# Kernel tuning notes

Hardware: AMD Instinct MI355X
Metric: run time of the kernel (lower is better)

## Reference

```python
import jax, jax.numpy as jnp
import numpy as np

B, S, D = 2, 2048, 1024
N_HEADS = 16
HEAD_DIM = D // N_HEADS  # 64, even for RoPE
THETA = 10000.0


def rope_tables(seq, head_dim, dtype=jnp.float32):
    half = head_dim // 2
    freqs = 1.0 / (THETA ** (jnp.arange(half, dtype=jnp.float32) / half))
    angles = jnp.arange(seq, dtype=jnp.float32)[:, None] * freqs[None, :]  # [S, half]
    return jnp.cos(angles).astype(dtype), jnp.sin(angles).astype(dtype)


def apply_rope_interleaved(x, cos, sin):
    # x: [b, h, s, d]; even/odd interleaving
    x_even = x[..., 0::2]
    x_odd = x[..., 1::2]
    r_even = x_even * cos - x_odd * sin
    r_odd = x_even * sin + x_odd * cos
    # interleave back: stack on last axis then reshape
    out = jnp.stack([r_even, r_odd], axis=-1).reshape(x.shape)
    return out


def setup_inputs() -> dict:
    key = jax.random.key(0)
    ks = jax.random.split(key, 6)
    scale = 1.0 / np.sqrt(D)
    return {
        "x": jax.random.normal(ks[0], (B, S, D), dtype=jnp.float32),
        "Wq": jax.random.normal(ks[1], (D, D), dtype=jnp.float32) * scale,
        "Wk": jax.random.normal(ks[2], (D, D), dtype=jnp.float32) * scale,
        "Wv": jax.random.normal(ks[3], (D, D), dtype=jnp.float32) * scale,
        "Wo": jax.random.normal(ks[4], (D, D), dtype=jnp.float32) * scale,
        "bo": jnp.zeros((D,), dtype=jnp.float32),
    }


def reference(x, Wq, Wk, Wv, Wo, bo):
    b, s, _ = x.shape
    # QKV projections (no bias), split heads -> [b, h, s, hd]
    def proj(W):
        return jnp.einsum('bsd,de->bse', x, W).reshape(b, s, N_HEADS, HEAD_DIM).transpose(0, 2, 1, 3)
    q, k, v = proj(Wq), proj(Wk), proj(Wv)

    cos, sin = rope_tables(s, HEAD_DIM, x.dtype)  # [s, hd//2]
    q = apply_rope_interleaved(q, cos, sin)
    k = apply_rope_interleaved(k, cos, sin)

    scale = 1.0 / jnp.sqrt(jnp.asarray(HEAD_DIM, dtype=x.dtype))
    scores = jnp.einsum('bhqd,bhkd->bhqk', q, k) * scale  # [b, h, s, s]
    causal = jnp.tril(jnp.ones((s, s), dtype=bool))
    scores = jnp.where(causal[None, None], scores, jnp.asarray(-jnp.inf, dtype=scores.dtype))
    attn = jax.nn.softmax(scores, axis=-1)
    ctx = jnp.einsum('bhqk,bhkd->bhqd', attn, v)  # [b, h, s, hd]
    ctx = ctx.transpose(0, 2, 1, 3).reshape(b, s, N_HEADS * HEAD_DIM)
    return jnp.einsum('bsd,de->bse', ctx, Wo) + bo
```

## Files before the change

kernel.cpp:

```cpp
#include <hip/hip_runtime.h>
#include <hip/hip_bf16.h>
#include <math.h>

constexpr int Bb   = 2;
constexpr int S    = 2048;
constexpr int D    = 1024;
constexpr int H    = 16;
constexpr int Dh   = 64;
constexpr int HALF = 32;
constexpr int M    = Bb * S;
constexpr int K    = 1024;
constexpr int N    = 1024;

typedef __attribute__((ext_vector_type(8))) short short8;
typedef __attribute__((ext_vector_type(4))) float f32x4;

__device__ __forceinline__ unsigned short f2bf(float f) {
    unsigned int u = __float_as_uint(f);
    unsigned int r = (u + 0x7fffu + ((u >> 16) & 1u)) >> 16;
    return (unsigned short)r;
}

__device__ __forceinline__ void gl_lds16(const unsigned short* g, unsigned short* lds_base) {
    __builtin_amdgcn_global_load_lds(
        (const __attribute__((address_space(1))) unsigned int*)g,
        (__attribute__((address_space(3))) unsigned int*)lds_base, 16, 0, 0);
}

__global__ __launch_bounds__(256) void prep_kernel(
    const float* __restrict__ x,
    const float* W0, const float* W1, const float* W2, const float* W3,
    unsigned short* __restrict__ xb,
    unsigned short* T0, unsigned short* T1, unsigned short* T2, unsigned short* T3,
    float* __restrict__ cosT, float* __restrict__ sinT)
{
    __shared__ float tile[64][65];
    const int bid = blockIdx.x;
    const int tid = threadIdx.x;

    if (bid < 256) {
        int idx = bid * 256 + tid;
        int s = idx >> 5;
        int i = idx & 31;
        double freq = exp(-(double)i * (log(10000.0) / 32.0));
        double ang  = (double)s * freq;
        cosT[idx] = (float)cos(ang);
        sinT[idx] = (float)sin(ang);
    } else if (bid < 256 + 4096) {
        size_t i = (size_t)(bid - 256) * 256 + tid;
        float4 v = *(const float4*)(x + i * 4);
        ushort4 pk;
        pk.x = f2bf(v.x); pk.y = f2bf(v.y); pk.z = f2bf(v.z); pk.w = f2bf(v.w);
        *(ushort4*)(xb + i * 4) = pk;
    } else {
        int wb = bid - 4352;
        int z  = wb >> 8;
        int rem = wb & 255;
        const float* W = (z == 0) ? W0 : (z == 1) ? W1 : (z == 2) ? W2 : W3;
        unsigned short* T = (z == 0) ? T0 : (z == 1) ? T1 : (z == 2) ? T2 : T3;
        const int bk = (rem >> 4) * 64;
        const int bn = (rem & 15) * 64;
        const int lr = tid >> 4;
        const int lc = (tid & 15) * 4;

        #pragma unroll
        for (int i = 0; i < 4; ++i) {
            int r = lr + i * 16;
            float4 v = *(const float4*)(W + (size_t)(bk + r) * N + bn + lc);
            tile[r][lc + 0] = v.x; tile[r][lc + 1] = v.y;
            tile[r][lc + 2] = v.z; tile[r][lc + 3] = v.w;
        }
        __syncthreads();
        #pragma unroll
        for (int i = 0; i < 4; ++i) {
            int nr = lr + i * 16;
            ushort4 pk;
            pk.x = f2bf(tile[lc + 0][nr]);
            pk.y = f2bf(tile[lc + 1][nr]);
            pk.z = f2bf(tile[lc + 2][nr]);
            pk.w = f2bf(tile[lc + 3][nr]);
            *(ushort4*)(T + (size_t)(bn + nr) * K + bk + lc) = pk;
        }
    }
}

__global__ __launch_bounds__(512, 2) void gemm_qkv_kernel(
    const unsigned short* __restrict__ A,
    const unsigned short* __restrict__ BT,
    unsigned short* outQ, unsigned short* outK, unsigned short* outV,
    const float* __restrict__ cosT, const float* __restrict__ sinT)
{
    constexpr int NT   = 32;
    constexpr int BUFS = 256 * 32;
    __shared__ __align__(16) unsigned short As[4 * BUFS];
    __shared__ __align__(16) unsigned short Bs[4 * BUFS];

    const int tid  = threadIdx.x;
    const int wid  = tid >> 6;
    const int lane = tid & 63;
    const int col  = lane & 15;
    const int quad = lane >> 4;
    const int wr   = wid >> 2;
    const int wc   = wid & 3;

    const int mbase = blockIdx.y * 256;
    const int nbase = blockIdx.x * 256;

    const int srow = lane >> 2;
    const int sch  = lane & 3;
    const unsigned short *pA0, *pA1, *pB0, *pB1;
    unsigned short *dA0, *dA1, *dB0, *dB1;
    {
        int r0 = wid * 16 + srow;
        int r1 = 128 + wid * 16 + srow;
        pA0 = A  + (size_t)(mbase + r0) * K + ((sch + (r0 >> 1)) & 3) * 8;
        pA1 = A  + (size_t)(mbase + r1) * K + ((sch + (r1 >> 1)) & 3) * 8;
        pB0 = BT + (size_t)(nbase + r0) * K + ((sch + (r0 >> 1)) & 3) * 8;
        pB1 = BT + (size_t)(nbase + r1) * K + ((sch + (r1 >> 1)) & 3) * 8;
        dA0 = &As[(wid * 16) * 32];
        dA1 = &As[(128 + wid * 16) * 32];
        dB0 = &Bs[(wid * 16) * 32];
        dB1 = &Bs[(128 + wid * 16) * 32];
    }

    int aoff[8], boff[4];
    #pragma unroll
    for (int f = 0; f < 8; ++f) {
        int r = wr * 128 + f * 16 + col;
        aoff[f] = r * 32 + ((quad - (r >> 1)) & 3) * 8;
    }
    #pragma unroll
    for (int n = 0; n < 4; ++n) {
        int r = wc * 64 + n * 16 + col;
        boff[n] = r * 32 + ((quad - (r >> 1)) & 3) * 8;
    }

    f32x4 acc[8][4];
    #pragma unroll
    for (int f = 0; f < 8; ++f)
        #pragma unroll
        for (int n = 0; n < 4; ++n) acc[f][n] = (f32x4)0.f;

    auto stageA = [&](int slot) {
        gl_lds16(pA0, dA0 + slot * BUFS); pA0 += 32;
        gl_lds16(pA1, dA1 + slot * BUFS); pA1 += 32;
    };
    auto stageB = [&](int slot) {
        gl_lds16(pB0, dB0 + slot * BUFS); pB0 += 32;
        gl_lds16(pB1, dB1 + slot * BUFS); pB1 += 32;
    };

    stageA(0); stageB(0);
    stageA(1); stageB(1);
    stageA(2); stageB(2);
    asm volatile("s_waitcnt vmcnt(8)" ::: "memory");
    __builtin_amdgcn_s_barrier();
    __builtin_amdgcn_sched_barrier(0);

    #pragma unroll 1
    for (int t = 0; t < NT; ++t) {
        const unsigned short* Ab = &As[(t & 3) * BUFS];
        const unsigned short* Bc = &Bs[(t & 3) * BUFS];
        const int nslot = (t + 3) & 3;
        short8 af[4], bf[4];

        #pragma unroll
        for (int i = 0; i < 4; ++i) af[i] = *(const short8*)&Ab[aoff[i]];
        #pragma unroll
        for (int n = 0; n < 4; ++n) bf[n] = *(const short8*)&Bc[boff[n]];
        if (t < NT - 3) stageA(nslot);
        __builtin_amdgcn_sched_barrier(0);
        __builtin_amdgcn_s_barrier();
        asm volatile("s_waitcnt lgkmcnt(0)" ::: "memory");
        __builtin_amdgcn_s_setprio(1);
        #pragma unroll
        for (int i = 0; i < 4; ++i)
            #pragma unroll
            for (int n = 0; n < 4; ++n)
                acc[i][n] = __builtin_amdgcn_mfma_f32_16x16x32_bf16(af[i], bf[n], acc[i][n], 0, 0, 0);
        __builtin_amdgcn_s_setprio(0);
        __builtin_amdgcn_sched_barrier(0);
        __builtin_amdgcn_s_barrier();
        __builtin_amdgcn_sched_barrier(0);

        #pragma unroll
        for (int i = 0; i < 4; ++i) af[i] = *(const short8*)&Ab[aoff[4 + i]];
        if (t < NT - 3) stageB(nslot);
        __builtin_amdgcn_sched_barrier(0);
        __builtin_amdgcn_s_barrier();
        asm volatile("s_waitcnt lgkmcnt(0)" ::: "memory");
        __builtin_amdgcn_s_setprio(1);
        #pragma unroll
        for (int i = 0; i < 4; ++i)
            #pragma unroll
            for (int n = 0; n < 4; ++n)
                acc[4 + i][n] = __builtin_amdgcn_mfma_f32_16x16x32_bf16(af[i], bf[n], acc[4 + i][n], 0, 0, 0);
        __builtin_amdgcn_s_setprio(0);
        if (t < NT - 3)       { asm volatile("s_waitcnt vmcnt(8)" ::: "memory"); }
        else if (t == NT - 3) { asm volatile("s_waitcnt vmcnt(4)" ::: "memory"); }
        else if (t == NT - 2) { asm volatile("s_waitcnt vmcnt(0)" ::: "memory"); }
        __builtin_amdgcn_s_barrier();
        __builtin_amdgcn_sched_barrier(0);
    }

    const int z = nbase >> 10;
    if (z < 2) {
        unsigned short* o = z ? outK : outQ;
        #pragma unroll
        for (int n = 0; n < 4; ++n) {
            int nl = (nbase & 1023) + wc * 64 + n * 16 + col;
            int h = nl >> 6, dh0 = nl & 63, p = dh0 >> 1;
            bool even = !(dh0 & 1);
            #pragma unroll
            for (int f = 0; f < 8; ++f)
                #pragma unroll
                for (int reg = 0; reg < 4; ++reg) {
                    int m_g = mbase + wr * 128 + f * 16 + quad * 4 + reg;
                    int b = m_g >> 11, s = m_g & 2047;
                    float v = acc[f][n][reg];
                    float part = __shfl_xor(v, 1, 64);
                    float c = cosT[s * HALF + p], sn = sinT[s * HALF + p];
                    float r = even ? (v * c - part * sn) : (v * c + part * sn);
                    o[((size_t)(b * H + h) * S + s) * Dh + dh0] = f2bf(r);
                }
        }
    } else {
        #pragma unroll
        for (int n = 0; n < 4; ++n) {
            int nl = (nbase & 1023) + wc * 64 + n * 16 + col;
            int h = nl >> 6, dh0 = nl & 63;
            #pragma unroll
            for (int f = 0; f < 8; ++f) {
                int m0 = mbase + wr * 128 + f * 16 + quad * 4;
                int b = m0 >> 11, s = m0 & 2047;
                ushort4 pk;
                pk.x = f2bf(acc[f][n][0]);
                pk.y = f2bf(acc[f][n][1]);
                pk.z = f2bf(acc[f][n][2]);
                pk.w = f2bf(acc[f][n][3]);
                *(ushort4*)&outV[((size_t)(b * H + h) * Dh + dh0) * S + s] = pk;
            }
        }
    }
}

__global__ __launch_bounds__(256) void gemm_out_kernel(
    const unsigned short* __restrict__ A,
    const unsigned short* __restrict__ BT,
    float* __restrict__ outO, const float* __restrict__ bias)
{
    constexpr int BK   = 64;
    constexpr int ABUF = 64 * BK;
    constexpr int BBUF = 64 * BK;
    __shared__ __align__(16) unsigned short As[2 * ABUF];
    __shared__ __align__(16) unsigned short Bs[2 * BBUF];

    const int tid  = threadIdx.x;
    const int wave = tid >> 6;
    const int lane = tid & 63;
    const int col  = lane & 15;
    const int quad = lane >> 4;
    const int wy   = wave >> 1;
    const int wx   = wave & 1;

    const int mbase = blockIdx.y * 64;
    const int nbase = blockIdx.x * 64;

    const int srow8 = lane >> 3;
    const int sch8  = lane & 7;

    const unsigned short *pA[2], *pB[2];
    unsigned short *dA[2], *dB[2];
    #pragma unroll
    for (int w = 0; w < 2; ++w) {
        int base = wave * 16 + w * 8;
        int tr = base + srow8;
        pA[w] = A  + (size_t)(mbase + tr) * K + ((sch8 + (tr >> 1)) & 7) * 8;
        pB[w] = BT + (size_t)(nbase + tr) * K + ((sch8 + (tr >> 1)) & 7) * 8;
        dA[w] = &As[base * BK];
        dB[w] = &Bs[base * BK];
    }

    int aoff[2][2], boff[2][2];
    #pragma unroll
    for (int ks = 0; ks < 2; ++ks) {
        #pragma unroll
        for (int mi = 0; mi < 2; ++mi) {
            int r = wy * 32 + mi * 16 + col;
            aoff[ks][mi] = r * BK + (((ks * 4 + quad) - (r >> 1)) & 7) * 8;
        }
        #pragma unroll
        for (int ni = 0; ni < 2; ++ni) {
            int r = wx * 32 + ni * 16 + col;
            boff[ks][ni] = r * BK + (((ks * 4 + quad) - (r >> 1)) & 7) * 8;
        }
    }

    f32x4 acc[2][2];
    #pragma unroll
    for (int mi = 0; mi < 2; ++mi)
        #pragma unroll
        for (int ni = 0; ni < 2; ++ni) acc[mi][ni] = (f32x4)0.f;

    auto stage = [&](int buf) {
        #pragma unroll
        for (int w = 0; w < 2; ++w) { gl_lds16(pA[w], dA[w] + buf * ABUF); pA[w] += BK; }
        #pragma unroll
        for (int w = 0; w < 2; ++w) { gl_lds16(pB[w], dB[w] + buf * BBUF); pB[w] += BK; }
    };
    auto compute = [&](int buf) {
        const unsigned short* Ac = &As[buf * ABUF];
        const unsigned short* Bc = &Bs[buf * BBUF];
        #pragma unroll
        for (int ks = 0; ks < 2; ++ks) {
            short8 af[2], bfr[2];
            #pragma unroll
            for (int mi = 0; mi < 2; ++mi) af[mi] = *(const short8*)&Ac[aoff[ks][mi]];
            #pragma unroll
            for (int ni = 0; ni < 2; ++ni) bfr[ni] = *(const short8*)&Bc[boff[ks][ni]];
            #pragma unroll
            for (int mi = 0; mi < 2; ++mi)
                #pragma unroll
                for (int ni = 0; ni < 2; ++ni)
                    acc[mi][ni] = __builtin_amdgcn_mfma_f32_16x16x32_bf16(af[mi], bfr[ni], acc[mi][ni], 0, 0, 0);
        }
    };

    stage(0);
    #pragma unroll 1
    for (int kk = 0; kk < 16; kk += 2) {
        __syncthreads();
        if (kk + 1 < 16) stage(1);
        compute(0);
        __syncthreads();
        if (kk + 2 < 16) stage(0);
        compute(1);
    }

    #pragma unroll
    for (int ni = 0; ni < 2; ++ni) {
        int n_g = nbase + wx * 32 + ni * 16 + col;
        float bv = bias[n_g];
        #pragma unroll
        for (int mi = 0; mi < 2; ++mi)
            #pragma unroll
            for (int reg = 0; reg < 4; ++reg) {
                int m_g = mbase + wy * 32 + mi * 16 + quad * 4 + reg;
                outO[(size_t)m_g * N + n_g] = acc[mi][ni][reg] + bv;
            }
    }
}

__global__ __launch_bounds__(256) void attn_mfma_kernel(
    const unsigned short* __restrict__ q, const unsigned short* __restrict__ k,
    const unsigned short* __restrict__ vt,
    float* __restrict__ Opart, float* __restrict__ lpart)
{
    constexpr int TSZ = 64 * 64;
    __shared__ __align__(16) unsigned short Ks[2 * TSZ];
    __shared__ __align__(16) unsigned short Vs[2 * TSZ];
    __shared__ __align__(16) unsigned short Ps[4][16 * 64];

    const int tid  = threadIdx.x;
    const int wave = tid >> 6;
    const int lane = tid & 63;
    const int col  = lane & 15;
    const int quad = lane >> 4;
    const int l8   = lane >> 3, cp = lane & 7;

    const int pairh = blockIdx.x;
    const int pair  = pairh >> 1;
    const int hpar  = pairh & 1;
    const int bh = blockIdx.y;
    const unsigned short* qb = q  + (size_t)bh * S * Dh;
    const unsigned short* kb = k  + (size_t)bh * S * Dh;
    const unsigned short* vb = vt + (size_t)bh * Dh * S;

    unsigned short* dk0 = &Ks[(wave * 16 + 0) * 64];
    unsigned short* dk1 = &Ks[(wave * 16 + 8) * 64];
    unsigned short* dv0 = &Vs[(wave * 16 + 0) * 64];
    unsigned short* dv1 = &Vs[(wave * 16 + 8) * 64];

    int foff[2][4];
    #pragma unroll
    for (int ks = 0; ks < 2; ++ks)
        #pragma unroll
        for (int nt = 0; nt < 4; ++nt) {
            int r = nt * 16 + col;
            foff[ks][nt] = r * 64 + (((ks * 4 + quad) - r) & 7) * 8;
        }
    int poffW[4][4];
    #pragma unroll
    for (int nt = 0; nt < 4; ++nt)
        #pragma unroll
        for (int reg = 0; reg < 4; ++reg) {
            int row = quad * 4 + reg;
            poffW[nt][reg] = row * 64 + (((nt * 2 + (col >> 3)) ^ (row & 7)) << 3) + (col & 7);
        }
    int poffR[2];
    #pragma unroll
    for (int ks = 0; ks < 2; ++ks)
        poffR[ks] = col * 64 + (((ks * 4 + quad) ^ (col & 7)) << 3);

    for (int phase = 0; phase < 2; ++phase) {
        const int qt  = phase ? (31 - pair) : pair;
        const int wr0 = qt * 64 + wave * 16;

        const unsigned short *pk0, *pk1, *pv0, *pv1;
        {
            int r0 = wave * 16 + l8, r1 = r0 + 8;
            pk0 = kb + (size_t)(hpar * 64 + r0) * Dh + ((cp + r0) & 7) * 8;
            pk1 = kb + (size_t)(hpar * 64 + r1) * Dh + ((cp + r1) & 7) * 8;
            pv0 = vb + (size_t)r0 * S + hpar * 64 + ((cp + r0) & 7) * 8;
            pv1 = vb + (size_t)r1 * S + hpar * 64 + ((cp + r1) & 7) * 8;
        }

        auto stageKV = [&](int buf) {
            gl_lds16(pk0, dk0 + buf * TSZ); gl_lds16(pk1, dk1 + buf * TSZ);
            gl_lds16(pv0, dv0 + buf * TSZ); gl_lds16(pv1, dv1 + buf * TSZ);
            pk0 += 128 * Dh; pk1 += 128 * Dh; pv0 += 128; pv1 += 128;
        };

        __syncthreads();
        if (hpar <= qt) stageKV(0);

        short8 qfrag[2];
        #pragma unroll
        for (int ks = 0; ks < 2; ++ks)
            qfrag[ks] = *(const short8*)(qb + (size_t)(wr0 + col) * Dh + ks * 32 + quad * 8);

        f32x4 O[4];
        float lacc[4];
        #pragma unroll
        for (int nt = 0; nt < 4; ++nt) O[nt] = (f32x4)0.f;
        #pragma unroll
        for (int r = 0; r < 4; ++r) lacc[r] = 0.f;

        auto subtile = [&](const unsigned short* Kc, const unsigned short* Vc, int t) {
            f32x4 sacc[4];
            #pragma unroll
            for (int nt = 0; nt < 4; ++nt) sacc[nt] = (f32x4)0.f;
            #pragma unroll
            for (int ks = 0; ks < 2; ++ks)
                #pragma unroll
                for (int nt = 0; nt < 4; ++nt) {
                    short8 kf = *(const short8*)&Kc[foff[ks][nt]];
                    sacc[nt] = __builtin_amdgcn_mfma_f32_16x16x32_bf16(qfrag[ks], kf, sacc[nt], 0, 0, 0);
                }
            float pb[4][4];
            #pragma unroll
            for (int nt = 0; nt < 4; ++nt) {
                int key_l = nt * 16 + col;
                #pragma unroll
                for (int reg = 0; reg < 4; ++reg) {
                    float e = __builtin_amdgcn_exp2f(
                        fmaf(sacc[nt][reg], 0.18033688011112042f, -11.541560327111707f));
                    if (t == qt && key_l > wave * 16 + quad * 4 + reg) e = 0.f;
                    pb[nt][reg] = e;
                }
            }
            #pragma unroll
            for (int reg = 0; reg < 4; ++reg)
                lacc[reg] += (pb[0][reg] + pb[1][reg]) + (pb[2][reg] + pb[3][reg]);
            #pragma unroll
            for (int nt = 0; nt < 4; ++nt)
                #pragma unroll
                for (int reg = 0; reg < 4; ++reg)
                    Ps[wave][poffW[nt][reg]] = f2bf(pb[nt][reg]);
            #pragma unroll
            for (int ks = 0; ks < 2; ++ks) {
                short8 pf = *(const short8*)&Ps[wave][poffR[ks]];
                #pragma unroll
                for (int nt = 0; nt < 4; ++nt) {
                    short8 vf = *(const short8*)&Vc[foff[ks][nt]];
                    O[nt] = __builtin_amdgcn_mfma_f32_16x16x32_bf16(pf, vf, O[nt], 0, 0, 0);
                }
            }
        };

        int j = 0;
        for (int i = hpar; i <= qt; i += 2, ++j) {
            __syncthreads();
            if (i + 2 <= qt) stageKV((j + 1) & 1);
            subtile(&Ks[(j & 1) * TSZ], &Vs[(j & 1) * TSZ], i);
        }

        #pragma unroll
        for (int reg = 0; reg < 4; ++reg) {
            float s = lacc[reg];
            #pragma unroll
            for (int off = 1; off <= 8; off <<= 1)
                s += __shfl_xor(s, off, 64);
            lacc[reg] = s;
        }

        const size_t pb_base = (size_t)(hpar * 32 + bh) * S;
        #pragma unroll
        for (int reg = 0; reg < 4; ++reg) {
            int rg = wr0 + quad * 4 + reg;
            float* op = Opart + (pb_base + rg) * 64 + col;
            #pragma unroll
            for (int nt = 0; nt < 4; ++nt)
                op[nt * 16] = O[nt][reg];
            if (col == 0)
                lpart[pb_base + rg] = lacc[reg];
        }
    }
}

__global__ __launch_bounds__(256) void combine_kernel(
    const float* __restrict__ Opart, const float* __restrict__ lpart,
    unsigned short* __restrict__ ctx)
{
    int gid = blockIdx.x * 256 + threadIdx.x;
    int bh  = gid >> 15;
    int rem = gid & 32767;
    int qr  = rem >> 4;
    int dg  = (rem & 15) << 2;

    size_t i0 = ((size_t)bh * S + qr) * 64 + dg;
    size_t i1 = ((size_t)(32 + bh) * S + qr) * 64 + dg;
    float4 a = *(const float4*)(Opart + i0);
    float4 c = *(const float4*)(Opart + i1);
    float inv = 1.0f / (lpart[(size_t)bh * S + qr] + lpart[(size_t)(32 + bh) * S + qr]);

    int b = bh >> 4, hh = bh & 15;
    ushort4 pk;
    pk.x = f2bf((a.x + c.x) * inv);
    pk.y = f2bf((a.y + c.y) * inv);
    pk.z = f2bf((a.z + c.z) * inv);
    pk.w = f2bf((a.w + c.w) * inv);
    *(ushort4*)(ctx + ((size_t)b * S + qr) * 1024 + hh * 64 + dg) = pk;
}

extern "C" void kernel_launch(void* const* d_in, const int* in_sizes, int n_in,
                              void* d_out, int out_size, void* d_ws, size_t ws_size,
                              hipStream_t stream) {
    const float* x  = (const float*)d_in[0];
    const float* Wq = (const float*)d_in[1];
    const float* Wk = (const float*)d_in[2];
    const float* Wv = (const float*)d_in[3];
    const float* Wo = (const float*)d_in[4];
    const float* bo = (const float*)d_in[5];
    float* out = (float*)d_out;

    const size_t MK  = (size_t)M * K;
    const size_t NK  = (size_t)N * K;
    const size_t QKV = (size_t)Bb * H * S * Dh;

    unsigned short* xb   = (unsigned short*)d_ws;
    unsigned short* WqT  = xb  + MK;
    unsigned short* WkT  = WqT + NK;
    unsigned short* WvT  = WkT + NK;
    unsigned short* WoT  = WvT + NK;
    unsigned short* qbuf = WoT + NK;
    unsigned short* kbuf = qbuf + QKV;
    unsigned short* vtb  = kbuf + QKV;
    unsigned short* ctxb = vtb  + QKV;
    float* cosT  = (float*)(ctxb + QKV);
    float* sinT  = cosT + (size_t)S * HALF;
    float* Opart = sinT + (size_t)S * HALF;
    float* lpart = Opart + (size_t)2 * 32 * S * 64;

    prep_kernel<<<5376, 256, 0, stream>>>(x, Wq, Wk, Wv, Wo,
                                          xb, WqT, WkT, WvT, WoT, cosT, sinT);

    gemm_qkv_kernel<<<dim3(12, 16), 512, 0, stream>>>(
        xb, WqT, qbuf, kbuf, vtb, cosT, sinT);

    attn_mfma_kernel<<<dim3(32, Bb * H), 256, 0, stream>>>(qbuf, kbuf, vtb, Opart, lpart);

    combine_kernel<<<4096, 256, 0, stream>>>(Opart, lpart, ctxb);

    gemm_out_kernel<<<dim3(16, 64), 256, 0, stream>>>(ctxb, WoT, out, bo);
}
```

Measured before the change: 188.8 us.

## Shrink QKV GEMM to 128x128 tiles with simple double buffering

Replaces the 256x256-tile, 512-thread QKV GEMM with 128x128 tiles, 256 threads and a plain two-buffer pipeline that uses __syncthreads. The old version had a 4-stage pipeline with hand-placed waitcnt, setprio and sched barriers. The grid grows from 192 to 768 blocks, which should fill the 256 CUs better and cut wave-quantization tail. In exchange, each block reuses less data per tile, and the loads no longer overlap compute as finely, so global and LDS traffic per FLOP rises.

```diff
diff --git a/kernel.cpp b/kernel.cpp
--- a/kernel.cpp
+++ b/kernel.cpp
@@ -84,140 +84,109 @@
     }
 }
 
-__global__ __launch_bounds__(512, 2) void gemm_qkv_kernel(
+__global__ __launch_bounds__(256) void gemm_qkv_kernel(
     const unsigned short* __restrict__ A,
     const unsigned short* __restrict__ BT,
     unsigned short* outQ, unsigned short* outK, unsigned short* outV,
     const float* __restrict__ cosT, const float* __restrict__ sinT)
 {
-    constexpr int NT   = 32;
-    constexpr int BUFS = 256 * 32;
-    __shared__ __align__(16) unsigned short As[4 * BUFS];
-    __shared__ __align__(16) unsigned short Bs[4 * BUFS];
+    constexpr int BUF = 128 * 32;
+    __shared__ __align__(16) unsigned short As[2 * BUF];
+    __shared__ __align__(16) unsigned short Bs[2 * BUF];
 
     const int tid  = threadIdx.x;
-    const int wid  = tid >> 6;
+    const int wave = tid >> 6;
     const int lane = tid & 63;
     const int col  = lane & 15;
     const int quad = lane >> 4;
-    const int wr   = wid >> 2;
-    const int wc   = wid & 3;
-
-    const int mbase = blockIdx.y * 256;
-    const int nbase = blockIdx.x * 256;
+    const int wy   = wave >> 1;
+    const int wx   = wave & 1;
+
+    const int mbase = blockIdx.y * 128;
+    const int nbase = blockIdx.x * 128;
 
     const int srow = lane >> 2;
     const int sch  = lane & 3;
     const unsigned short *pA0, *pA1, *pB0, *pB1;
     unsigned short *dA0, *dA1, *dB0, *dB1;
     {
-        int r0 = wid * 16 + srow;
-        int r1 = 128 + wid * 16 + srow;
+        int r0 = wave * 32 + srow;
+        int r1 = wave * 32 + 16 + srow;
         pA0 = A  + (size_t)(mbase + r0) * K + ((sch + (r0 >> 1)) & 3) * 8;
         pA1 = A  + (size_t)(mbase + r1) * K + ((sch + (r1 >> 1)) & 3) * 8;
         pB0 = BT + (size_t)(nbase + r0) * K + ((sch + (r0 >> 1)) & 3) * 8;
         pB1 = BT + (size_t)(nbase + r1) * K + ((sch + (r1 >> 1)) & 3) * 8;
-        dA0 = &As[(wid * 16) * 32];
-        dA1 = &As[(128 + wid * 16) * 32];
-        dB0 = &Bs[(wid * 16) * 32];
-        dB1 = &Bs[(128 + wid * 16) * 32];
-    }
-
-    int aoff[8], boff[4];
-    #pragma unroll
-    for (int f = 0; f < 8; ++f) {
-        int r = wr * 128 + f * 16 + col;
-        aoff[f] = r * 32 + ((quad - (r >> 1)) & 3) * 8;
-    }
-    #pragma unroll
-    for (int n = 0; n < 4; ++n) {
-        int r = wc * 64 + n * 16 + col;
-        boff[n] = r * 32 + ((quad - (r >> 1)) & 3) * 8;
-    }
-
-    f32x4 acc[8][4];
-    #pragma unroll
-    for (int f = 0; f < 8; ++f)
-        #pragma unroll
-        for (int n = 0; n < 4; ++n) acc[f][n] = (f32x4)0.f;
-
-    auto stageA = [&](int slot) {
-        gl_lds16(pA0, dA0 + slot * BUFS); pA0 += 32;
-        gl_lds16(pA1, dA1 + slot * BUFS); pA1 += 32;
+        dA0 = &As[(wave * 32) * 32];
+        dA1 = &As[(wave * 32 + 16) * 32];
+        dB0 = &Bs[(wave * 32) * 32];
+        dB1 = &Bs[(wave * 32 + 16) * 32];
+    }
+
+    int aoff[4], boff[4];
+    #pragma unroll
+    for (int mi = 0; mi < 4; ++mi) {
+        int r = wy * 64 + mi * 16 + col;
+        aoff[mi] = r * 32 + ((quad - (r >> 1)) & 3) * 8;
+    }
+    #pragma unroll
+    for (int ni = 0; ni < 4; ++ni) {
+        int r = wx * 64 + ni * 16 + col;
+        boff[ni] = r * 32 + ((quad - (r >> 1)) & 3) * 8;
+    }
+
+    f32x4 acc[4][4];
+    #pragma unroll
+    for (int mi = 0; mi < 4; ++mi)
+        #pragma unroll
+        for (int ni = 0; ni < 4; ++ni) acc[mi][ni] = (f32x4)0.f;
+
+    auto stage = [&](int buf) {
+        gl_lds16(pA0, dA0 + buf * BUF);  pA0 += 32;
+        gl_lds16(pA1, dA1 + buf * BUF);  pA1 += 32;
+        gl_lds16(pB0, dB0 + buf * BUF);  pB0 += 32;
+        gl_lds16(pB1, dB1 + buf * BUF);  pB1 += 32;
     };
-    auto stageB = [&](int slot) {
-        gl_lds16(pB0, dB0 + slot * BUFS); pB0 += 32;
-        gl_lds16(pB1, dB1 + slot * BUFS); pB1 += 32;
+    auto compute = [&](int buf) {
+        const unsigned short* Ac = &As[buf * BUF];
+        const unsigned short* Bc = &Bs[buf * BUF];
+        short8 af[4], bfr[4];
+        #pragma unroll
+        for (int mi = 0; mi < 4; ++mi) af[mi] = *(const short8*)&Ac[aoff[mi]];
+        #pragma unroll
+        for (int ni = 0; ni < 4; ++ni) bfr[ni] = *(const short8*)&Bc[boff[ni]];
+        #pragma unroll
+        for (int mi = 0; mi < 4; ++mi)
+            #pragma unroll
+            for (int ni = 0; ni < 4; ++ni)
+                acc[mi][ni] = __builtin_amdgcn_mfma_f32_16x16x32_bf16(af[mi], bfr[ni], acc[mi][ni], 0, 0, 0);
     };
 
-    stageA(0); stageB(0);
-    stageA(1); stageB(1);
-    stageA(2); stageB(2);
-    asm volatile("s_waitcnt vmcnt(8)" ::: "memory");
-    __builtin_amdgcn_s_barrier();
-    __builtin_amdgcn_sched_barrier(0);
-
+    stage(0);
     #pragma unroll 1
-    for (int t = 0; t < NT; ++t) {
-        const unsigned short* Ab = &As[(t & 3) * BUFS];
-        const unsigned short* Bc = &Bs[(t & 3) * BUFS];
-        const int nslot = (t + 3) & 3;
-        short8 af[4], bf[4];
-
-        #pragma unroll
-        for (int i = 0; i < 4; ++i) af[i] = *(const short8*)&Ab[aoff[i]];
-        #pragma unroll
-        for (int n = 0; n < 4; ++n) bf[n] = *(const short8*)&Bc[boff[n]];
-        if (t < NT - 3) stageA(nslot);
-        __builtin_amdgcn_sched_barrier(0);
-        __builtin_amdgcn_s_barrier();
-        asm volatile("s_waitcnt lgkmcnt(0)" ::: "memory");
-        __builtin_amdgcn_s_setprio(1);
-        #pragma unroll
-        for (int i = 0; i < 4; ++i)
-            #pragma unroll
-            for (int n = 0; n < 4; ++n)
-                acc[i][n] = __builtin_amdgcn_mfma_f32_16x16x32_bf16(af[i], bf[n], acc[i][n], 0, 0, 0);
-        __builtin_amdgcn_s_setprio(0);
-        __builtin_amdgcn_sched_barrier(0);
-        __builtin_amdgcn_s_barrier();
-        __builtin_amdgcn_sched_barrier(0);
-
-        #pragma unroll
-        for (int i = 0; i < 4; ++i) af[i] = *(const short8*)&Ab[aoff[4 + i]];
-        if (t < NT - 3) stageB(nslot);
-        __builtin_amdgcn_sched_barrier(0);
-        __builtin_amdgcn_s_barrier();
-        asm volatile("s_waitcnt lgkmcnt(0)" ::: "memory");
-        __builtin_amdgcn_s_setprio(1);
-        #pragma unroll
-        for (int i = 0; i < 4; ++i)
-            #pragma unroll
-            for (int n = 0; n < 4; ++n)
-                acc[4 + i][n] = __builtin_amdgcn_mfma_f32_16x16x32_bf16(af[i], bf[n], acc[4 + i][n], 0, 0, 0);
-        __builtin_amdgcn_s_setprio(0);
-        if (t < NT - 3)       { asm volatile("s_waitcnt vmcnt(8)" ::: "memory"); }
-        else if (t == NT - 3) { asm volatile("s_waitcnt vmcnt(4)" ::: "memory"); }
-        else if (t == NT - 2) { asm volatile("s_waitcnt vmcnt(0)" ::: "memory"); }
-        __builtin_amdgcn_s_barrier();
-        __builtin_amdgcn_sched_barrier(0);
+    for (int kk = 0; kk < 32; kk += 2) {
+        __syncthreads();
+        if (kk + 1 < 32) stage(1);
+        compute(0);
+        __syncthreads();
+        if (kk + 2 < 32) stage(0);
+        compute(1);
     }
 
     const int z = nbase >> 10;
     if (z < 2) {
         unsigned short* o = z ? outK : outQ;
         #pragma unroll
-        for (int n = 0; n < 4; ++n) {
-            int nl = (nbase & 1023) + wc * 64 + n * 16 + col;
+        for (int ni = 0; ni < 4; ++ni) {
+            int nl = (nbase & 1023) + wx * 64 + ni * 16 + col;
             int h = nl >> 6, dh0 = nl & 63, p = dh0 >> 1;
             bool even = !(dh0 & 1);
             #pragma unroll
-            for (int f = 0; f < 8; ++f)
+            for (int mi = 0; mi < 4; ++mi)
                 #pragma unroll
                 for (int reg = 0; reg < 4; ++reg) {
-                    int m_g = mbase + wr * 128 + f * 16 + quad * 4 + reg;
+                    int m_g = mbase + wy * 64 + mi * 16 + quad * 4 + reg;
                     int b = m_g >> 11, s = m_g & 2047;
-                    float v = acc[f][n][reg];
+                    float v = acc[mi][ni][reg];
                     float part = __shfl_xor(v, 1, 64);
                     float c = cosT[s * HALF + p], sn = sinT[s * HALF + p];
                     float r = even ? (v * c - part * sn) : (v * c + part * sn);
@@ -226,18 +195,18 @@
         }
     } else {
         #pragma unroll
-        for (int n = 0; n < 4; ++n) {
-            int nl = (nbase & 1023) + wc * 64 + n * 16 + col;
+        for (int ni = 0; ni < 4; ++ni) {
+            int nl = (nbase & 1023) + wx * 64 + ni * 16 + col;
             int h = nl >> 6, dh0 = nl & 63;
             #pragma unroll
-            for (int f = 0; f < 8; ++f) {
-                int m0 = mbase + wr * 128 + f * 16 + quad * 4;
+            for (int mi = 0; mi < 4; ++mi) {
+                int m0 = mbase + wy * 64 + mi * 16 + quad * 4;
                 int b = m0 >> 11, s = m0 & 2047;
                 ushort4 pk;
-                pk.x = f2bf(acc[f][n][0]);
-                pk.y = f2bf(acc[f][n][1]);
-                pk.z = f2bf(acc[f][n][2]);
-                pk.w = f2bf(acc[f][n][3]);
+                pk.x = f2bf(acc[mi][ni][0]);
+                pk.y = f2bf(acc[mi][ni][1]);
+                pk.z = f2bf(acc[mi][ni][2]);
+                pk.w = f2bf(acc[mi][ni][3]);
                 *(ushort4*)&outV[((size_t)(b * H + h) * Dh + dh0) * S + s] = pk;
             }
         }
@@ -565,7 +534,7 @@
     prep_kernel<<<5376, 256, 0, stream>>>(x, Wq, Wk, Wv, Wo,
                                           xb, WqT, WkT, WvT, WoT, cosT, sinT);
 
-    gemm_qkv_kernel<<<dim3(12, 16), 512, 0, stream>>>(
+    gemm_qkv_kernel<<<dim3(24, 32), 256, 0, stream>>>(
         xb, WqT, qbuf, kbuf, vtb, cosT, sinT);
 
     attn_mfma_kernel<<<dim3(32, Bb * H), 256, 0, stream>>>(qbuf, kbuf, vtb, Opart, lpart);
```

Result: slower. 199.3 us (+5.6%).

## Retile QKV GEMM to 256x192 tiles with K=64 double buffering

Applied to the files above, without the earlier changes.

The QKV projection GEMM now uses 256x192 output tiles instead of 256x256, so the grid grows from 192 to 256 workgroups and better fills the GPU's compute units. The K step doubles to 64 per stage with two LDS slots instead of a four-deep ring of K=32 slots, and the swizzle is widened to 8 chunks. Because the tile no longer lines up with the Q/K/V 1024 boundaries, the epilogue picks the output and RoPE path per column group. The shallower pipeline waits for all loads (vmcnt(0)) each iteration, which may expose more memory latency.

```diff
diff --git a/kernel.cpp b/kernel.cpp
--- a/kernel.cpp
+++ b/kernel.cpp
@@ -90,10 +90,11 @@
     unsigned short* outQ, unsigned short* outK, unsigned short* outV,
     const float* __restrict__ cosT, const float* __restrict__ sinT)
 {
-    constexpr int NT   = 32;
-    constexpr int BUFS = 256 * 32;
-    __shared__ __align__(16) unsigned short As[4 * BUFS];
-    __shared__ __align__(16) unsigned short Bs[4 * BUFS];
+    constexpr int NT    = 16;
+    constexpr int ASLOT = 256 * 64;
+    constexpr int BSLOT = 192 * 64;
+    __shared__ __align__(16) unsigned short As[2 * ASLOT];
+    __shared__ __align__(16) unsigned short Bs[2 * BSLOT];
 
     const int tid  = threadIdx.x;
     const int wid  = tid >> 6;
@@ -104,71 +105,72 @@
     const int wc   = wid & 3;
 
     const int mbase = blockIdx.y * 256;
-    const int nbase = blockIdx.x * 256;
-
-    const int srow = lane >> 2;
-    const int sch  = lane & 3;
-    const unsigned short *pA0, *pA1, *pB0, *pB1;
-    unsigned short *dA0, *dA1, *dB0, *dB1;
-    {
-        int r0 = wid * 16 + srow;
-        int r1 = 128 + wid * 16 + srow;
-        pA0 = A  + (size_t)(mbase + r0) * K + ((sch + (r0 >> 1)) & 3) * 8;
-        pA1 = A  + (size_t)(mbase + r1) * K + ((sch + (r1 >> 1)) & 3) * 8;
-        pB0 = BT + (size_t)(nbase + r0) * K + ((sch + (r0 >> 1)) & 3) * 8;
-        pB1 = BT + (size_t)(nbase + r1) * K + ((sch + (r1 >> 1)) & 3) * 8;
-        dA0 = &As[(wid * 16) * 32];
-        dA1 = &As[(128 + wid * 16) * 32];
-        dB0 = &Bs[(wid * 16) * 32];
-        dB1 = &Bs[(128 + wid * 16) * 32];
-    }
-
-    int aoff[8], boff[4];
-    #pragma unroll
-    for (int f = 0; f < 8; ++f) {
-        int r = wr * 128 + f * 16 + col;
-        aoff[f] = r * 32 + ((quad - (r >> 1)) & 3) * 8;
-    }
-    #pragma unroll
-    for (int n = 0; n < 4; ++n) {
-        int r = wc * 64 + n * 16 + col;
-        boff[n] = r * 32 + ((quad - (r >> 1)) & 3) * 8;
-    }
-
-    f32x4 acc[8][4];
+    const int nbase = blockIdx.x * 192;
+
+    const int srow8 = lane >> 3;
+    const int sch8  = lane & 7;
+    const unsigned short *pA[4], *pB[3];
+    unsigned short *dA[4], *dB[3];
+    #pragma unroll
+    for (int w = 0; w < 4; ++w) {
+        int r = wid * 32 + w * 8 + srow8;
+        pA[w] = A + (size_t)(mbase + r) * K + ((sch8 + (r >> 1)) & 7) * 8;
+        dA[w] = &As[(wid * 32 + w * 8) * 64];
+    }
+    #pragma unroll
+    for (int w = 0; w < 3; ++w) {
+        int r = wid * 24 + w * 8 + srow8;
+        pB[w] = BT + (size_t)(nbase + r) * K + ((sch8 + (r >> 1)) & 7) * 8;
+        dB[w] = &Bs[(wid * 24 + w * 8) * 64];
+    }
+
+    int aoff[2][8], boff[2][3];
+    #pragma unroll
+    for (int kh = 0; kh < 2; ++kh) {
+        #pragma unroll
+        for (int f = 0; f < 8; ++f) {
+            int r = wr * 128 + f * 16 + col;
+            aoff[kh][f] = r * 64 + (((kh * 4 + quad) - (r >> 1)) & 7) * 8;
+        }
+        #pragma unroll
+        for (int n = 0; n < 3; ++n) {
+            int r = wc * 48 + n * 16 + col;
+            boff[kh][n] = r * 64 + (((kh * 4 + quad) - (r >> 1)) & 7) * 8;
+        }
+    }
+
+    f32x4 acc[8][3];
     #pragma unroll
     for (int f = 0; f < 8; ++f)
         #pragma unroll
-        for (int n = 0; n < 4; ++n) acc[f][n] = (f32x4)0.f;
+        for (int n = 0; n < 3; ++n) acc[f][n] = (f32x4)0.f;
 
     auto stageA = [&](int slot) {
-        gl_lds16(pA0, dA0 + slot * BUFS); pA0 += 32;
-        gl_lds16(pA1, dA1 + slot * BUFS); pA1 += 32;
+        #pragma unroll
+        for (int w = 0; w < 4; ++w) { gl_lds16(pA[w], dA[w] + slot * ASLOT); pA[w] += 64; }
     };
     auto stageB = [&](int slot) {
-        gl_lds16(pB0, dB0 + slot * BUFS); pB0 += 32;
-        gl_lds16(pB1, dB1 + slot * BUFS); pB1 += 32;
+        #pragma unroll
+        for (int w = 0; w < 3; ++w) { gl_lds16(pB[w], dB[w] + slot * BSLOT); pB[w] += 64; }
     };
 
     stageA(0); stageB(0);
-    stageA(1); stageB(1);
-    stageA(2); stageB(2);
-    asm volatile("s_waitcnt vmcnt(8)" ::: "memory");
+    asm volatile("s_waitcnt vmcnt(0)" ::: "memory");
     __builtin_amdgcn_s_barrier();
     __builtin_amdgcn_sched_barrier(0);
 
     #pragma unroll 1
     for (int t = 0; t < NT; ++t) {
-        const unsigned short* Ab = &As[(t & 3) * BUFS];
-        const unsigned short* Bc = &Bs[(t & 3) * BUFS];
-        const int nslot = (t + 3) & 3;
-        short8 af[4], bf[4];
-
-        #pragma unroll
-        for (int i = 0; i < 4; ++i) af[i] = *(const short8*)&Ab[aoff[i]];
-        #pragma unroll
-        for (int n = 0; n < 4; ++n) bf[n] = *(const short8*)&Bc[boff[n]];
-        if (t < NT - 3) stageA(nslot);
+        const unsigned short* Ab = &As[(t & 1) * ASLOT];
+        const unsigned short* Bc = &Bs[(t & 1) * BSLOT];
+        const int ns = (t + 1) & 1;
+        short8 af[4], bf[3];
+
+        #pragma unroll
+        for (int i = 0; i < 4; ++i) af[i] = *(const short8*)&Ab[aoff[0][i]];
+        #pragma unroll
+        for (int n = 0; n < 3; ++n) bf[n] = *(const short8*)&Bc[boff[0][n]];
+        if (t < NT - 1) stageA(ns);
         __builtin_amdgcn_sched_barrier(0);
         __builtin_amdgcn_s_barrier();
         asm volatile("s_waitcnt lgkmcnt(0)" ::: "memory");
@@ -176,7 +178,7 @@
         #pragma unroll
         for (int i = 0; i < 4; ++i)
             #pragma unroll
-            for (int n = 0; n < 4; ++n)
+            for (int n = 0; n < 3; ++n)
                 acc[i][n] = __builtin_amdgcn_mfma_f32_16x16x32_bf16(af[i], bf[n], acc[i][n], 0, 0, 0);
         __builtin_amdgcn_s_setprio(0);
         __builtin_amdgcn_sched_barrier(0);
@@ -184,8 +186,8 @@
         __builtin_amdgcn_sched_barrier(0);
 
         #pragma unroll
-        for (int i = 0; i < 4; ++i) af[i] = *(const short8*)&Ab[aoff[4 + i]];
-        if (t < NT - 3) stageB(nslot);
+        for (int i = 0; i < 4; ++i) af[i] = *(const short8*)&Ab[aoff[0][4 + i]];
+        if (t < NT - 1) stageB(ns);
         __builtin_amdgcn_sched_barrier(0);
         __builtin_amdgcn_s_barrier();
         asm volatile("s_waitcnt lgkmcnt(0)" ::: "memory");
@@ -193,23 +195,58 @@
         #pragma unroll
         for (int i = 0; i < 4; ++i)
             #pragma unroll
-            for (int n = 0; n < 4; ++n)
+            for (int n = 0; n < 3; ++n)
                 acc[4 + i][n] = __builtin_amdgcn_mfma_f32_16x16x32_bf16(af[i], bf[n], acc[4 + i][n], 0, 0, 0);
         __builtin_amdgcn_s_setprio(0);
-        if (t < NT - 3)       { asm volatile("s_waitcnt vmcnt(8)" ::: "memory"); }
-        else if (t == NT - 3) { asm volatile("s_waitcnt vmcnt(4)" ::: "memory"); }
-        else if (t == NT - 2) { asm volatile("s_waitcnt vmcnt(0)" ::: "memory"); }
-        __builtin_amdgcn_s_barrier();
-        __builtin_amdgcn_sched_barrier(0);
-    }
-
-    const int z = nbase >> 10;
-    if (z < 2) {
-        unsigned short* o = z ? outK : outQ;
-        #pragma unroll
-        for (int n = 0; n < 4; ++n) {
-            int nl = (nbase & 1023) + wc * 64 + n * 16 + col;
-            int h = nl >> 6, dh0 = nl & 63, p = dh0 >> 1;
+        __builtin_amdgcn_sched_barrier(0);
+        __builtin_amdgcn_s_barrier();
+        __builtin_amdgcn_sched_barrier(0);
+
+        #pragma unroll
+        for (int i = 0; i < 4; ++i) af[i] = *(const short8*)&Ab[aoff[1][i]];
+        #pragma unroll
+        for (int n = 0; n < 3; ++n) bf[n] = *(const short8*)&Bc[boff[1][n]];
+        __builtin_amdgcn_sched_barrier(0);
+        __builtin_amdgcn_s_barrier();
+        asm volatile("s_waitcnt lgkmcnt(0)" ::: "memory");
+        __builtin_amdgcn_s_setprio(1);
+        #pragma unroll
+        for (int i = 0; i < 4; ++i)
+            #pragma unroll
+            for (int n = 0; n < 3; ++n)
+                acc[i][n] = __builtin_amdgcn_mfma_f32_16x16x32_bf16(af[i], bf[n], acc[i][n], 0, 0, 0);
+        __builtin_amdgcn_s_setprio(0);
+        __builtin_amdgcn_sched_barrier(0);
+        __builtin_amdgcn_s_barrier();
+        __builtin_amdgcn_sched_barrier(0);
+
+        #pragma unroll
+        for (int i = 0; i < 4; ++i) af[i] = *(const short8*)&Ab[aoff[1][4 + i]];
+        __builtin_amdgcn_sched_barrier(0);
+        __builtin_amdgcn_s_barrier();
+        asm volatile("s_waitcnt lgkmcnt(0)" ::: "memory");
+        __builtin_amdgcn_s_setprio(1);
+        #pragma unroll
+        for (int i = 0; i < 4; ++i)
+            #pragma unroll
+            for (int n = 0; n < 3; ++n)
+                acc[4 + i][n] = __builtin_amdgcn_mfma_f32_16x16x32_bf16(af[i], bf[n], acc[4 + i][n], 0, 0, 0);
+        __builtin_amdgcn_s_setprio(0);
+        if (t < NT - 1) { asm volatile("s_waitcnt vmcnt(0)" ::: "memory"); }
+        __builtin_amdgcn_sched_barrier(0);
+        __builtin_amdgcn_s_barrier();
+        __builtin_amdgcn_sched_barrier(0);
+    }
+
+    #pragma unroll
+    for (int n = 0; n < 3; ++n) {
+        int n_g = nbase + wc * 48 + n * 16 + col;
+        int z   = n_g >> 10;
+        int nl  = n_g & 1023;
+        int h = nl >> 6, dh0 = nl & 63;
+        if (z < 2) {
+            unsigned short* o = z ? outK : outQ;
+            int p = dh0 >> 1;
             bool even = !(dh0 & 1);
             #pragma unroll
             for (int f = 0; f < 8; ++f)
@@ -223,12 +260,7 @@
                     float r = even ? (v * c - part * sn) : (v * c + part * sn);
                     o[((size_t)(b * H + h) * S + s) * Dh + dh0] = f2bf(r);
                 }
-        }
-    } else {
-        #pragma unroll
-        for (int n = 0; n < 4; ++n) {
-            int nl = (nbase & 1023) + wc * 64 + n * 16 + col;
-            int h = nl >> 6, dh0 = nl & 63;
+        } else {
             #pragma unroll
             for (int f = 0; f < 8; ++f) {
                 int m0 = mbase + wr * 128 + f * 16 + quad * 4;
@@ -565,7 +597,7 @@
     prep_kernel<<<5376, 256, 0, stream>>>(x, Wq, Wk, Wv, Wo,
                                           xb, WqT, WkT, WvT, WoT, cosT, sinT);
 
-    gemm_qkv_kernel<<<dim3(12, 16), 512, 0, stream>>>(
+    gemm_qkv_kernel<<<dim3(16, 16), 512, 0, stream>>>(
         xb, WqT, qbuf, kbuf, vtb, cosT, sinT);
 
     attn_mfma_kernel<<<dim3(32, Bb * H), 256, 0, stream>>>(qbuf, kbuf, vtb, Opart, lpart);
```

Result: no change. 190.0 us (+0.6%).
